# Kernel optimization log

Hardware: AMD Instinct MI355X
Metric: run time of the kernel (lower is better)

## Reference

```python
import jax, jax.numpy as jnp
import numpy as np

N, T1, T2 = 150000, 30000, 8192
E1, E2 = 400000, 160000
F_IN, F_HID, F_OUT = 512, 256, 20


def setup_inputs() -> dict:
    key = jax.random.key(0)
    ks = jax.random.split(key, 10)
    return {
        "x": jax.random.normal(ks[0], (N, F_IN), dtype=jnp.float32),
        "src1": jax.random.randint(ks[1], (E1,), 0, N, dtype=jnp.int32),
        "dst1": jax.random.randint(ks[2], (E1,), 0, T1, dtype=jnp.int32),
        "src2": jax.random.randint(ks[3], (E2,), 0, T1, dtype=jnp.int32),
        "dst2": jax.random.randint(ks[4], (E2,), 0, T2, dtype=jnp.int32),
        "Wl1": jax.random.normal(ks[5], (F_HID, F_IN), dtype=jnp.float32) * 0.05,
        "bl1": jnp.zeros((F_HID,), dtype=jnp.float32),
        "Wr1": jax.random.normal(ks[6], (F_HID, F_IN), dtype=jnp.float32) * 0.05,
        "Wl2": jax.random.normal(ks[7], (F_OUT, F_HID), dtype=jnp.float32) * 0.05,
        "bl2": jnp.zeros((F_OUT,), dtype=jnp.float32),
        "Wr2": jax.random.normal(ks[8], (F_OUT, F_HID), dtype=jnp.float32) * 0.05,
    }


def _sage_conv(x_src, x_tgt, src, dst, num_tgt, Wl, bl, Wr):
    # PyG SAGEConv (mean aggr, root_weight=True, bias on lin_l):
    # out = lin_l(mean_{j in N(i)} x_src[j]) + lin_r(x_tgt[i])
    msg = x_src[src]                                                  # [E, F]
    agg = jax.ops.segment_sum(msg, dst, num_segments=num_tgt)        # [T, F]
    cnt = jax.ops.segment_sum(jnp.ones((src.shape[0],), x_src.dtype), dst,
                              num_segments=num_tgt)                  # [T]
    mean = agg / jnp.maximum(cnt, 1.0)[:, None]
    return mean @ Wl.T + bl + x_tgt @ Wr.T


def reference(x, src1, dst1, src2, dst2, Wl1, bl1, Wr1, Wl2, bl2, Wr2):
    # Layer 1: [N, F_IN] -> [T1, F_HID], relu (eval mode: no dropout)
    h = _sage_conv(x, x[:T1], src1, dst1, T1, Wl1, bl1, Wr1)
    h = jax.nn.relu(h)
    # Layer 2: [T1, F_HID] -> [T2, F_OUT]
    out = _sage_conv(h, h[:T2], src2, dst2, T2, Wl2, bl2, Wr2)
    return jax.nn.log_softmax(out, axis=-1)
```

## Files before the change

kernel.cpp:

```cpp
#include <hip/hip_runtime.h>
#include <math.h>

constexpr int T1N  = 30000;
constexpr int T2N  = 8192;
constexpr int FIN  = 512;
constexpr int FHID = 256;
constexpr int FOUT = 20;
constexpr int NPAD = 32;

typedef short bf16x8 __attribute__((ext_vector_type(8)));
typedef short bf16x4 __attribute__((ext_vector_type(4)));
typedef float f32x4  __attribute__((ext_vector_type(4)));

__device__ __forceinline__ short f2bf(float f) {
    unsigned u = __float_as_uint(f);
    u += 0x7fff + ((u >> 16) & 1);
    return (short)(u >> 16);
}
__device__ __forceinline__ float bf2f(short s) {
    return __uint_as_float(((unsigned)(unsigned short)s) << 16);
}

__device__ __forceinline__ void gload16(const void* g, void* l) {
    __builtin_amdgcn_global_load_lds(
        (const __attribute__((address_space(1))) void*)g,
        (__attribute__((address_space(3))) void*)l, 16, 0, 0);
}

__global__ void count_both(const int* __restrict__ dst1, const int* __restrict__ dst2,
        int* __restrict__ cnt1, int* __restrict__ cnt2, int E1, int E2) {
    int i = blockIdx.x * blockDim.x + threadIdx.x;
    int stride = gridDim.x * blockDim.x;
    int tot = E1 + E2;
    for (; i < tot; i += stride) {
        if (i < E1) atomicAdd(&cnt1[dst1[i]], 1);
        else        atomicAdd(&cnt2[dst2[i - E1]], 1);
    }
}

__global__ __launch_bounds__(1024) void scan_both(
        const int* __restrict__ cnt1, int* __restrict__ rs1, int* __restrict__ cur1,
        const int* __restrict__ cnt2, int* __restrict__ rs2, int* __restrict__ cur2) {
    const int* cnt = (blockIdx.x == 0) ? cnt1 : cnt2;
    int* rs  = (blockIdx.x == 0) ? rs1  : rs2;
    int* cur = (blockIdx.x == 0) ? cur1 : cur2;
    int T    = (blockIdx.x == 0) ? T1N  : T2N;
    __shared__ int wsum[16];
    int tid = threadIdx.x;
    int lane = tid & 63, wid = tid >> 6;
    int carry = 0;
    for (int base = 0; base < T; base += 4096) {
        int i = base + tid * 4;
        int4 v = make_int4(0, 0, 0, 0);
        if (i + 3 < T) v = *(const int4*)(cnt + i);
        else {
            if (i     < T) v.x = cnt[i];
            if (i + 1 < T) v.y = cnt[i + 1];
            if (i + 2 < T) v.z = cnt[i + 2];
        }
        int tsum = v.x + v.y + v.z + v.w;
        int s = tsum;
        #pragma unroll
        for (int off = 1; off < 64; off <<= 1) {
            int t = __shfl_up(s, off, 64);
            if (lane >= off) s += t;
        }
        if (lane == 63) wsum[wid] = s;
        __syncthreads();
        if (wid == 0) {
            int w = (lane < 16) ? wsum[lane] : 0;
            #pragma unroll
            for (int off = 1; off < 16; off <<= 1) {
                int t = __shfl_up(w, off, 64);
                if (lane >= off) w += t;
            }
            if (lane < 16) wsum[lane] = w;
        }
        __syncthreads();
        int e0 = s - tsum + (wid > 0 ? wsum[wid - 1] : 0) + carry;
        int e1 = e0 + v.x, e2 = e1 + v.y, e3 = e2 + v.z;
        if (i + 3 < T) {
            *(int4*)(rs + i)  = make_int4(e0, e1, e2, e3);
            *(int4*)(cur + i) = make_int4(e0, e1, e2, e3);
        } else {
            if (i     < T) { rs[i]     = e0; cur[i]     = e0; }
            if (i + 1 < T) { rs[i + 1] = e1; cur[i + 1] = e1; }
            if (i + 2 < T) { rs[i + 2] = e2; cur[i + 2] = e2; }
        }
        int total = wsum[15];
        __syncthreads();
        carry += total;
    }
    if (tid == 0) rs[T] = carry;
}

__global__ void scatter_both(const int* __restrict__ src1, const int* __restrict__ dst1,
        const int* __restrict__ src2, const int* __restrict__ dst2,
        int* __restrict__ cur1, int* __restrict__ cur2,
        int* __restrict__ ss1, int* __restrict__ ss2, int E1, int E2) {
    int i = blockIdx.x * blockDim.x + threadIdx.x;
    int stride = gridDim.x * blockDim.x;
    int tot = E1 + E2;
    for (; i < tot; i += stride) {
        if (i < E1) {
            int pos = atomicAdd(&cur1[dst1[i]], 1);
            ss1[pos] = src1[i];
        } else {
            int j = i - E1;
            int pos = atomicAdd(&cur2[dst2[j]], 1);
            ss2[pos] = src2[j];
        }
    }
}

__global__ void convert_x_full(const float* __restrict__ x, short* __restrict__ xbf, long n8) {
    long i = ((long)blockIdx.x * blockDim.x + threadIdx.x);
    if (i >= n8) return;
    const float* p = x + i * 8;
    float4 v0 = *(const float4*)p;
    float4 v1 = *(const float4*)(p + 4);
    bf16x8 o;
    o[0] = f2bf(v0.x); o[1] = f2bf(v0.y); o[2] = f2bf(v0.z); o[3] = f2bf(v0.w);
    o[4] = f2bf(v1.x); o[5] = f2bf(v1.y); o[6] = f2bf(v1.z); o[7] = f2bf(v1.w);
    *(bf16x8*)(xbf + i * 8) = o;
}

__global__ void convert_w_all(const float* __restrict__ Wl1, const float* __restrict__ Wr1,
        const float* __restrict__ Wl2, short* __restrict__ Wl1bf,
        short* __restrict__ Wr1bf, short* __restrict__ Wl2pad) {
    int i = (blockIdx.x * blockDim.x + threadIdx.x) * 8;
    const int S1 = FHID * FIN;
    if (i < S1) {
        const float* sp = Wl1 + i;
        float4 v0 = *(const float4*)sp, v1 = *(const float4*)(sp + 4);
        bf16x8 o;
        o[0]=f2bf(v0.x); o[1]=f2bf(v0.y); o[2]=f2bf(v0.z); o[3]=f2bf(v0.w);
        o[4]=f2bf(v1.x); o[5]=f2bf(v1.y); o[6]=f2bf(v1.z); o[7]=f2bf(v1.w);
        *(bf16x8*)(Wl1bf + i) = o;
    } else if (i < 2 * S1) {
        const float* sp = Wr1 + (i - S1);
        float4 v0 = *(const float4*)sp, v1 = *(const float4*)(sp + 4);
        bf16x8 o;
        o[0]=f2bf(v0.x); o[1]=f2bf(v0.y); o[2]=f2bf(v0.z); o[3]=f2bf(v0.w);
        o[4]=f2bf(v1.x); o[5]=f2bf(v1.y); o[6]=f2bf(v1.z); o[7]=f2bf(v1.w);
        *(bf16x8*)(Wr1bf + (i - S1)) = o;
    } else if (i < 2 * S1 + NPAD * FHID) {
        int k = i - 2 * S1;
        int row = k >> 8;
        bf16x8 o;
        if (row < FOUT) {
            const float* sp = Wl2 + (size_t)row * FHID + (k & 255);
            float4 v0 = *(const float4*)sp, v1 = *(const float4*)(sp + 4);
            o[0]=f2bf(v0.x); o[1]=f2bf(v0.y); o[2]=f2bf(v0.z); o[3]=f2bf(v0.w);
            o[4]=f2bf(v1.x); o[5]=f2bf(v1.y); o[6]=f2bf(v1.z); o[7]=f2bf(v1.w);
        } else {
            o = (bf16x8)(short)0;
        }
        *(bf16x8*)(Wl2pad + k) = o;
    }
}

template <int MODE>
__global__ __launch_bounds__(256, 2) void gemm_l1(
        const short* __restrict__ A, const short* __restrict__ W,
        const float* __restrict__ bias, void* __restrict__ outv, int M) {
    __shared__ short As[2][128 * 32];
    __shared__ short Bs[2][256 * 32];
    int tid = threadIdx.x;
    int wid = tid >> 6, lane = tid & 63;
    int brow = blockIdx.x * 128;
    int wr = (wid >> 1) * 64, wc = (wid & 1) * 128;

    f32x4 acc[4][8] = {};
    int kgrp = lane >> 4;
    int r16 = lane & 15;

    auto stage = [&](int buf, int kt) {
        #pragma unroll
        for (int c2 = 0; c2 < 2; ++c2) {
            int q = wid + c2 * 4;
            int c = q * 64 + lane;
            int row = c >> 2;
            int sl = (c & 3) ^ ((row ^ (row >> 2)) & 3);
            int gr = brow + row; if (gr > M - 1) gr = M - 1;
            gload16(A + (size_t)gr * 512 + kt + sl * 8, (char*)As[buf] + q * 1024);
        }
        #pragma unroll
        for (int c2 = 0; c2 < 4; ++c2) {
            int q = wid + c2 * 4;
            int c = q * 64 + lane;
            int row = c >> 2;
            int sl = (c & 3) ^ ((row ^ (row >> 2)) & 3);
            gload16(W + (size_t)row * 512 + kt + sl * 8, (char*)Bs[buf] + q * 1024);
        }
    };

    stage(0, 0);
    __syncthreads();

    int cur = 0;
    for (int kt = 0; kt < 512; kt += 32) {
        if (kt + 32 < 512) stage(cur ^ 1, kt + 32);

        bf16x8 af[4], bfr[8];
        #pragma unroll
        for (int m = 0; m < 4; ++m) {
            int row = wr + m * 16 + r16;
            int sl = kgrp ^ ((row ^ (row >> 2)) & 3);
            af[m] = *(const bf16x8*)((const char*)As[cur] + row * 64 + sl * 16);
        }
        #pragma unroll
        for (int n = 0; n < 8; ++n) {
            int row = wc + n * 16 + r16;
            int sl = kgrp ^ ((row ^ (row >> 2)) & 3);
            bfr[n] = *(const bf16x8*)((const char*)Bs[cur] + row * 64 + sl * 16);
        }
        #pragma unroll
        for (int m = 0; m < 4; ++m)
            #pragma unroll
            for (int n = 0; n < 8; ++n)
                acc[m][n] = __builtin_amdgcn_mfma_f32_16x16x32_bf16(
                        af[m], bfr[n], acc[m][n], 0, 0, 0);

        __syncthreads();
        cur ^= 1;
    }

    int g4 = lane >> 4;
    #pragma unroll
    for (int n = 0; n < 8; ++n) {
        int col = wc + n * 16 + r16;
        float bv = (MODE == 1) ? bias[col] : 0.f;
        #pragma unroll
        for (int m = 0; m < 4; ++m) {
            #pragma unroll
            for (int r = 0; r < 4; ++r) {
                int row = brow + wr + m * 16 + g4 * 4 + r;
                if (row < M) {
                    if (MODE == 0)
                        ((short*)outv)[(size_t)row * 256 + col] = f2bf(acc[m][n][r]);
                    else
                        ((float*)outv)[(size_t)row * 256 + col] = acc[m][n][r] + bv;
                }
            }
        }
    }
}

__global__ void agg1_kernel(const short* __restrict__ y, const int* __restrict__ ss,
        const int* __restrict__ rs, const float* __restrict__ hr,
        float* __restrict__ h, short* __restrict__ hbf, int T) {
    int gw = (int)((blockIdx.x * (size_t)blockDim.x + threadIdx.x) >> 6);
    int lane = threadIdx.x & 63;
    if (gw >= T) return;
    int j0 = rs[gw], j1 = rs[gw + 1];
    float a[4] = {};
    for (int j = j0; j < j1; ++j) {
        int s = ss[j];
        bf16x4 v = *(const bf16x4*)(y + (size_t)s * FHID + lane * 4);
        a[0] += bf2f(v[0]); a[1] += bf2f(v[1]); a[2] += bf2f(v[2]); a[3] += bf2f(v[3]);
    }
    int d = j1 - j0;
    float inv = 1.0f / (float)(d > 1 ? d : 1);
    float4 hv = *(const float4*)(hr + (size_t)gw * FHID + lane * 4);
    float o0 = fmaxf(a[0] * inv + hv.x, 0.f);
    float o1 = fmaxf(a[1] * inv + hv.y, 0.f);
    float o2 = fmaxf(a[2] * inv + hv.z, 0.f);
    float o3 = fmaxf(a[3] * inv + hv.w, 0.f);
    *(float4*)(h + (size_t)gw * FHID + lane * 4) = make_float4(o0, o1, o2, o3);
    bf16x4 ob; ob[0] = f2bf(o0); ob[1] = f2bf(o1); ob[2] = f2bf(o2); ob[3] = f2bf(o3);
    *(bf16x4*)(hbf + (size_t)gw * FHID + lane * 4) = ob;
}

__global__ __launch_bounds__(128, 2) void gemm_z(
        const short* __restrict__ A, const short* __restrict__ W,
        float* __restrict__ z, int M) {
    __shared__ short As[2][128 * 32];
    __shared__ short Bs[2][32 * 32];
    int tid = threadIdx.x;
    int wid = tid >> 6, lane = tid & 63;
    int brow = blockIdx.x * 128;
    int wr = wid * 64;

    f32x4 acc[4][2] = {};
    int kgrp = lane >> 4;
    int r16 = lane & 15;

    auto stage = [&](int buf, int kt) {
        #pragma unroll
        for (int c2 = 0; c2 < 4; ++c2) {
            int q = wid + c2 * 2;
            int c = q * 64 + lane;
            int row = c >> 2;
            int sl = (c & 3) ^ ((row ^ (row >> 2)) & 3);
            int gr = brow + row; if (gr > M - 1) gr = M - 1;
            gload16(A + (size_t)gr * 256 + kt + sl * 8, (char*)As[buf] + q * 1024);
        }
        {
            int q = wid;
            int c = q * 64 + lane;
            int row = c >> 2;
            int sl = (c & 3) ^ ((row ^ (row >> 2)) & 3);
            gload16(W + (size_t)row * 256 + kt + sl * 8, (char*)Bs[buf] + q * 1024);
        }
    };

    stage(0, 0);
    __syncthreads();

    int cur = 0;
    for (int kt = 0; kt < 256; kt += 32) {
        if (kt + 32 < 256) stage(cur ^ 1, kt + 32);

        bf16x8 af[4], bfr[2];
        #pragma unroll
        for (int m = 0; m < 4; ++m) {
            int row = wr + m * 16 + r16;
            int sl = kgrp ^ ((row ^ (row >> 2)) & 3);
            af[m] = *(const bf16x8*)((const char*)As[cur] + row * 64 + sl * 16);
        }
        #pragma unroll
        for (int n = 0; n < 2; ++n) {
            int row = n * 16 + r16;
            int sl = kgrp ^ ((row ^ (row >> 2)) & 3);
            bfr[n] = *(const bf16x8*)((const char*)Bs[cur] + row * 64 + sl * 16);
        }
        #pragma unroll
        for (int m = 0; m < 4; ++m)
            #pragma unroll
            for (int n = 0; n < 2; ++n)
                acc[m][n] = __builtin_amdgcn_mfma_f32_16x16x32_bf16(
                        af[m], bfr[n], acc[m][n], 0, 0, 0);

        __syncthreads();
        cur ^= 1;
    }

    int g4 = lane >> 4;
    #pragma unroll
    for (int n = 0; n < 2; ++n) {
        int col = n * 16 + r16;
        #pragma unroll
        for (int m = 0; m < 4; ++m) {
            #pragma unroll
            for (int r = 0; r < 4; ++r) {
                int row = brow + wr + m * 16 + g4 * 4 + r;
                if (row < M)
                    z[(size_t)row * NPAD + col] = acc[m][n][r];
            }
        }
    }
}

__global__ void agg2z_kernel(const float* __restrict__ z, const int* __restrict__ ss,
        const int* __restrict__ rs, float* __restrict__ mz, int T) {
    int gw = (int)((blockIdx.x * (size_t)blockDim.x + threadIdx.x) >> 6);
    int lane = threadIdx.x & 63;
    int t = gw * 2 + (lane >> 5);
    int c = lane & 31;
    if (t >= T) return;
    int j0 = rs[t], j1 = rs[t + 1];
    float a = 0.f;
    for (int j = j0; j < j1; ++j)
        a += z[(size_t)ss[j] * NPAD + c];
    int d = j1 - j0;
    mz[(size_t)t * NPAD + c] = a / (float)(d > 1 ? d : 1);
}

__global__ __launch_bounds__(256) void lsm_kernel(const float* __restrict__ mz,
        const float* __restrict__ h, const float* __restrict__ Wr,
        const float* __restrict__ bias, float* __restrict__ out) {
    __shared__ float Wrs[FOUT * FHID];
    int tid = threadIdx.x;
    for (int i = tid; i < FOUT * FHID / 4; i += 256)
        ((float4*)Wrs)[i] = ((const float4*)Wr)[i];
    __syncthreads();

    int row = blockIdx.x * 4 + (tid >> 6);
    int lane = tid & 63;
    if (row >= T2N) return;

    float acc[FOUT];
    #pragma unroll
    for (int o = 0; o < FOUT; ++o) acc[o] = 0.f;

    const float* hrow = h + (size_t)row * FHID;
    #pragma unroll
    for (int kk = 0; kk < 4; ++kk) {
        int k = lane + kk * 64;
        float hv = hrow[k];
        #pragma unroll
        for (int o = 0; o < FOUT; ++o)
            acc[o] = fmaf(hv, Wrs[o * FHID + k], acc[o]);
    }
    #pragma unroll
    for (int o = 0; o < FOUT; ++o)
        #pragma unroll
        for (int off = 32; off > 0; off >>= 1)
            acc[o] += __shfl_down(acc[o], off, 64);

    if (lane == 0) {
        float mx = -1e30f;
        #pragma unroll
        for (int o = 0; o < FOUT; ++o) {
            acc[o] += mz[(size_t)row * NPAD + o] + bias[o];
            mx = fmaxf(mx, acc[o]);
        }
        float s = 0.f;
        #pragma unroll
        for (int o = 0; o < FOUT; ++o) s += expf(acc[o] - mx);
        float lse = mx + logf(s);
        float* op = out + (size_t)row * FOUT;
        #pragma unroll
        for (int o = 0; o < FOUT; ++o) op[o] = acc[o] - lse;
    }
}

extern "C" void kernel_launch(void* const* d_in, const int* in_sizes, int n_in,
                              void* d_out, int out_size, void* d_ws, size_t ws_size,
                              hipStream_t stream) {
    const float* x   = (const float*)d_in[0];
    const int* src1  = (const int*)d_in[1];
    const int* dst1  = (const int*)d_in[2];
    const int* src2  = (const int*)d_in[3];
    const int* dst2  = (const int*)d_in[4];
    const float* Wl1 = (const float*)d_in[5];
    const float* bl1 = (const float*)d_in[6];
    const float* Wr1 = (const float*)d_in[7];
    const float* Wl2 = (const float*)d_in[8];
    const float* bl2 = (const float*)d_in[9];
    const float* Wr2 = (const float*)d_in[10];
    int E1 = in_sizes[1];
    int E2 = in_sizes[3];
    int N  = in_sizes[0] / FIN;

    char* p = (char*)d_ws;
    auto alloc = [&](size_t bytes) {
        char* r = p;
        p += (bytes + 255) & ~(size_t)255;
        return r;
    };
    short* xbf    = (short*)alloc((size_t)N * FIN * 2);
    short* ybuf   = (short*)alloc((size_t)N * FHID * 2);
    float* hr     = (float*)alloc((size_t)T1N * FHID * 4);
    float* hbuf   = (float*)alloc((size_t)T1N * FHID * 4);
    short* hbf    = (short*)alloc((size_t)T1N * FHID * 2);
    float* zbuf   = (float*)alloc((size_t)T1N * NPAD * 4);
    float* mz     = (float*)alloc((size_t)T2N * NPAD * 4);
    short* Wl1bf  = (short*)alloc((size_t)FHID * FIN * 2);
    short* Wr1bf  = (short*)alloc((size_t)FHID * FIN * 2);
    short* Wl2pad = (short*)alloc((size_t)NPAD * FHID * 2);
    int* cnt1 = (int*)alloc((size_t)T1N * 4);
    int* cnt2 = (int*)alloc((size_t)T2N * 4);
    int* rs1  = (int*)alloc((size_t)(T1N + 1) * 4);
    int* cur1 = (int*)alloc((size_t)T1N * 4);
    int* ss1  = (int*)alloc((size_t)E1 * 4);
    int* rs2  = (int*)alloc((size_t)(T2N + 1) * 4);
    int* cur2 = (int*)alloc((size_t)T2N * 4);
    int* ss2  = (int*)alloc((size_t)E2 * 4);

    hipMemsetAsync(cnt1, 0, (size_t)((char*)(cnt2 + T2N) - (char*)cnt1), stream);

    count_both<<<768, 256, 0, stream>>>(dst1, dst2, cnt1, cnt2, E1, E2);
    scan_both<<<2, 1024, 0, stream>>>(cnt1, rs1, cur1, cnt2, rs2, cur2);
    scatter_both<<<768, 256, 0, stream>>>(src1, dst1, src2, dst2, cur1, cur2, ss1, ss2, E1, E2);

    convert_w_all<<<((2 * FHID * FIN + NPAD * FHID) / 8 + 255) / 256, 256, 0, stream>>>(
        Wl1, Wr1, Wl2, Wl1bf, Wr1bf, Wl2pad);
    long n8 = (long)N * FIN / 8;
    convert_x_full<<<(int)((n8 + 255) / 256), 256, 0, stream>>>(x, xbf, n8);

    gemm_l1<1><<<(T1N + 127) / 128, 256, 0, stream>>>(xbf, Wr1bf, bl1, hr, T1N);
    gemm_l1<0><<<(N + 127) / 128, 256, 0, stream>>>(xbf, Wl1bf, nullptr, ybuf, N);
    agg1_kernel<<<(T1N * 64 + 255) / 256, 256, 0, stream>>>(ybuf, ss1, rs1, hr, hbuf, hbf, T1N);

    gemm_z<<<(T1N + 127) / 128, 128, 0, stream>>>(hbf, Wl2pad, zbuf, T1N);
    agg2z_kernel<<<(T2N / 2 * 64 + 255) / 256, 256, 0, stream>>>(zbuf, ss2, rs2, mz, T2N);
    lsm_kernel<<<T2N / 4, 256, 0, stream>>>(mz, hbuf, Wr2, bl2, (float*)d_out);
}
```

Baseline: 728.3 us.

## Aggregate raw features before layer-1 GEMM and fuse both weights into one K=1024 GEMM

Layer 1 now computes the neighbour mean directly on the bf16 input features for the 30000 target rows. It then runs a single MFMA GEMM over the concatenation [mean | x_tgt] against concatenated [Wl1 | Wr1] weights, with bias and ReLU fused into the epilogue. The old path transformed all 150000 source rows by Wl1, wrote a projected buffer and gathered from it. This removes most of the layer-1 GEMM work, the projected-buffer write and a separate pass. The cost is that each edge now gathers 512-wide bf16 rows instead of 256-wide ones, doubling per-edge gather traffic.

```diff
diff --git a/kernel.cpp b/kernel.cpp
--- a/kernel.cpp
+++ b/kernel.cpp
@@ -126,26 +126,22 @@
 }
 
 __global__ void convert_w_all(const float* __restrict__ Wl1, const float* __restrict__ Wr1,
-        const float* __restrict__ Wl2, short* __restrict__ Wl1bf,
-        short* __restrict__ Wr1bf, short* __restrict__ Wl2pad) {
+        const float* __restrict__ Wl2, short* __restrict__ Wcat,
+        short* __restrict__ Wl2pad) {
     int i = (blockIdx.x * blockDim.x + threadIdx.x) * 8;
-    const int S1 = FHID * FIN;
-    if (i < S1) {
-        const float* sp = Wl1 + i;
+    const int SC = FHID * 1024;
+    if (i < SC) {
+        int n = i >> 10;
+        int k = i & 1023;
+        const float* sp = (k < 512) ? (Wl1 + (size_t)n * FIN + k)
+                                    : (Wr1 + (size_t)n * FIN + (k - 512));
         float4 v0 = *(const float4*)sp, v1 = *(const float4*)(sp + 4);
         bf16x8 o;
         o[0]=f2bf(v0.x); o[1]=f2bf(v0.y); o[2]=f2bf(v0.z); o[3]=f2bf(v0.w);
         o[4]=f2bf(v1.x); o[5]=f2bf(v1.y); o[6]=f2bf(v1.z); o[7]=f2bf(v1.w);
-        *(bf16x8*)(Wl1bf + i) = o;
-    } else if (i < 2 * S1) {
-        const float* sp = Wr1 + (i - S1);
-        float4 v0 = *(const float4*)sp, v1 = *(const float4*)(sp + 4);
-        bf16x8 o;
-        o[0]=f2bf(v0.x); o[1]=f2bf(v0.y); o[2]=f2bf(v0.z); o[3]=f2bf(v0.w);
-        o[4]=f2bf(v1.x); o[5]=f2bf(v1.y); o[6]=f2bf(v1.z); o[7]=f2bf(v1.w);
-        *(bf16x8*)(Wr1bf + (i - S1)) = o;
-    } else if (i < 2 * S1 + NPAD * FHID) {
-        int k = i - 2 * S1;
+        *(bf16x8*)(Wcat + i) = o;
+    } else if (i < SC + NPAD * FHID) {
+        int k = i - SC;
         int row = k >> 8;
         bf16x8 o;
         if (row < FOUT) {
@@ -160,38 +156,63 @@
     }
 }
 
-template <int MODE>
-__global__ __launch_bounds__(256, 2) void gemm_l1(
-        const short* __restrict__ A, const short* __restrict__ W,
-        const float* __restrict__ bias, void* __restrict__ outv, int M) {
+__global__ void agg1_kernel(const short* __restrict__ xbf, const int* __restrict__ ss,
+        const int* __restrict__ rs, short* __restrict__ meanbf, int T) {
+    int gw = (int)((blockIdx.x * (size_t)blockDim.x + threadIdx.x) >> 6);
+    int lane = threadIdx.x & 63;
+    if (gw >= T) return;
+    int j0 = rs[gw], j1 = rs[gw + 1];
+    float a[8] = {};
+    int j = j0;
+    for (; j + 1 < j1; j += 2) {
+        int s0 = ss[j], s1 = ss[j + 1];
+        bf16x8 v0 = *(const bf16x8*)(xbf + (size_t)s0 * FIN + lane * 8);
+        bf16x8 v1 = *(const bf16x8*)(xbf + (size_t)s1 * FIN + lane * 8);
+        #pragma unroll
+        for (int q = 0; q < 8; ++q) a[q] += bf2f(v0[q]) + bf2f(v1[q]);
+    }
+    if (j < j1) {
+        int s0 = ss[j];
+        bf16x8 v0 = *(const bf16x8*)(xbf + (size_t)s0 * FIN + lane * 8);
+        #pragma unroll
+        for (int q = 0; q < 8; ++q) a[q] += bf2f(v0[q]);
+    }
+    int d = j1 - j0;
+    float inv = 1.0f / (float)(d > 1 ? d : 1);
+    bf16x8 o;
+    #pragma unroll
+    for (int q = 0; q < 8; ++q) o[q] = f2bf(a[q] * inv);
+    *(bf16x8*)(meanbf + (size_t)gw * FIN + lane * 8) = o;
+}
+
+__global__ __launch_bounds__(256, 2) void gemm1_mfma(
+        const short* __restrict__ Am, const short* __restrict__ Ax,
+        const short* __restrict__ W, const float* __restrict__ bias,
+        float* __restrict__ h, short* __restrict__ hbf) {
     __shared__ short As[2][128 * 32];
-    __shared__ short Bs[2][256 * 32];
+    __shared__ short Bs[2][128 * 32];
     int tid = threadIdx.x;
     int wid = tid >> 6, lane = tid & 63;
-    int brow = blockIdx.x * 128;
-    int wr = (wid >> 1) * 64, wc = (wid & 1) * 128;
-
-    f32x4 acc[4][8] = {};
+    int brow = blockIdx.x * 128, bcol = blockIdx.y * 128;
+    int wr = (wid >> 1) * 64, wc = (wid & 1) * 64;
+
+    f32x4 acc[4][4] = {};
     int kgrp = lane >> 4;
     int r16 = lane & 15;
 
     auto stage = [&](int buf, int kt) {
+        const short* Abase = (kt < 512) ? Am : Ax;
+        int ko = kt & 511;
         #pragma unroll
         for (int c2 = 0; c2 < 2; ++c2) {
             int q = wid + c2 * 4;
             int c = q * 64 + lane;
             int row = c >> 2;
-            int sl = (c & 3) ^ ((row ^ (row >> 2)) & 3);
-            int gr = brow + row; if (gr > M - 1) gr = M - 1;
-            gload16(A + (size_t)gr * 512 + kt + sl * 8, (char*)As[buf] + q * 1024);
-        }
-        #pragma unroll
-        for (int c2 = 0; c2 < 4; ++c2) {
-            int q = wid + c2 * 4;
-            int c = q * 64 + lane;
-            int row = c >> 2;
-            int sl = (c & 3) ^ ((row ^ (row >> 2)) & 3);
-            gload16(W + (size_t)row * 512 + kt + sl * 8, (char*)Bs[buf] + q * 1024);
+            int rx = (row ^ (row >> 2)) & 3;
+            int sl = (c & 3) ^ rx;
+            int gr = brow + row; if (gr > T1N - 1) gr = T1N - 1;
+            gload16(Abase + (size_t)gr * 512 + ko + sl * 8, (char*)As[buf] + q * 1024);
+            gload16(W + (size_t)(bcol + row) * 1024 + kt + sl * 8, (char*)Bs[buf] + q * 1024);
         }
     };
 
@@ -199,10 +220,10 @@
     __syncthreads();
 
     int cur = 0;
-    for (int kt = 0; kt < 512; kt += 32) {
-        if (kt + 32 < 512) stage(cur ^ 1, kt + 32);
-
-        bf16x8 af[4], bfr[8];
+    for (int kt = 0; kt < 1024; kt += 32) {
+        if (kt + 32 < 1024) stage(cur ^ 1, kt + 32);
+
+        bf16x8 af[4], bfr[4];
         #pragma unroll
         for (int m = 0; m < 4; ++m) {
             int row = wr + m * 16 + r16;
@@ -210,7 +231,7 @@
             af[m] = *(const bf16x8*)((const char*)As[cur] + row * 64 + sl * 16);
         }
         #pragma unroll
-        for (int n = 0; n < 8; ++n) {
+        for (int n = 0; n < 4; ++n) {
             int row = wc + n * 16 + r16;
             int sl = kgrp ^ ((row ^ (row >> 2)) & 3);
             bfr[n] = *(const bf16x8*)((const char*)Bs[cur] + row * 64 + sl * 16);
@@ -218,7 +239,7 @@
         #pragma unroll
         for (int m = 0; m < 4; ++m)
             #pragma unroll
-            for (int n = 0; n < 8; ++n)
+            for (int n = 0; n < 4; ++n)
                 acc[m][n] = __builtin_amdgcn_mfma_f32_16x16x32_bf16(
                         af[m], bfr[n], acc[m][n], 0, 0, 0);
 
@@ -228,48 +249,23 @@
 
     int g4 = lane >> 4;
     #pragma unroll
-    for (int n = 0; n < 8; ++n) {
-        int col = wc + n * 16 + r16;
-        float bv = (MODE == 1) ? bias[col] : 0.f;
+    for (int n = 0; n < 4; ++n) {
+        int col = bcol + wc + n * 16 + r16;
+        float bv = bias[col];
         #pragma unroll
         for (int m = 0; m < 4; ++m) {
             #pragma unroll
             for (int r = 0; r < 4; ++r) {
                 int row = brow + wr + m * 16 + g4 * 4 + r;
-                if (row < M) {
-                    if (MODE == 0)
-                        ((short*)outv)[(size_t)row * 256 + col] = f2bf(acc[m][n][r]);
-                    else
-                        ((float*)outv)[(size_t)row * 256 + col] = acc[m][n][r] + bv;
+                if (row < T1N) {
+                    float v = acc[m][n][r] + bv;
+                    v = v > 0.f ? v : 0.f;
+                    h[(size_t)row * FHID + col] = v;
+                    hbf[(size_t)row * FHID + col] = f2bf(v);
                 }
             }
         }
     }
-}
-
-__global__ void agg1_kernel(const short* __restrict__ y, const int* __restrict__ ss,
-        const int* __restrict__ rs, const float* __restrict__ hr,
-        float* __restrict__ h, short* __restrict__ hbf, int T) {
-    int gw = (int)((blockIdx.x * (size_t)blockDim.x + threadIdx.x) >> 6);
-    int lane = threadIdx.x & 63;
-    if (gw >= T) return;
-    int j0 = rs[gw], j1 = rs[gw + 1];
-    float a[4] = {};
-    for (int j = j0; j < j1; ++j) {
-        int s = ss[j];
-        bf16x4 v = *(const bf16x4*)(y + (size_t)s * FHID + lane * 4);
-        a[0] += bf2f(v[0]); a[1] += bf2f(v[1]); a[2] += bf2f(v[2]); a[3] += bf2f(v[3]);
-    }
-    int d = j1 - j0;
-    float inv = 1.0f / (float)(d > 1 ? d : 1);
-    float4 hv = *(const float4*)(hr + (size_t)gw * FHID + lane * 4);
-    float o0 = fmaxf(a[0] * inv + hv.x, 0.f);
-    float o1 = fmaxf(a[1] * inv + hv.y, 0.f);
-    float o2 = fmaxf(a[2] * inv + hv.z, 0.f);
-    float o3 = fmaxf(a[3] * inv + hv.w, 0.f);
-    *(float4*)(h + (size_t)gw * FHID + lane * 4) = make_float4(o0, o1, o2, o3);
-    bf16x4 ob; ob[0] = f2bf(o0); ob[1] = f2bf(o1); ob[2] = f2bf(o2); ob[3] = f2bf(o3);
-    *(bf16x4*)(hbf + (size_t)gw * FHID + lane * 4) = ob;
 }
 
 __global__ __launch_bounds__(128, 2) void gemm_z(
@@ -441,14 +437,12 @@
         return r;
     };
     short* xbf    = (short*)alloc((size_t)N * FIN * 2);
-    short* ybuf   = (short*)alloc((size_t)N * FHID * 2);
-    float* hr     = (float*)alloc((size_t)T1N * FHID * 4);
+    short* meanbf = (short*)alloc((size_t)T1N * FIN * 2);
     float* hbuf   = (float*)alloc((size_t)T1N * FHID * 4);
     short* hbf    = (short*)alloc((size_t)T1N * FHID * 2);
     float* zbuf   = (float*)alloc((size_t)T1N * NPAD * 4);
     float* mz     = (float*)alloc((size_t)T2N * NPAD * 4);
-    short* Wl1bf  = (short*)alloc((size_t)FHID * FIN * 2);
-    short* Wr1bf  = (short*)alloc((size_t)FHID * FIN * 2);
+    short* Wcat   = (short*)alloc((size_t)FHID * 1024 * 2);
     short* Wl2pad = (short*)alloc((size_t)NPAD * FHID * 2);
     int* cnt1 = (int*)alloc((size_t)T1N * 4);
     int* cnt2 = (int*)alloc((size_t)T2N * 4);
@@ -465,14 +459,14 @@
     scan_both<<<2, 1024, 0, stream>>>(cnt1, rs1, cur1, cnt2, rs2, cur2);
     scatter_both<<<768, 256, 0, stream>>>(src1, dst1, src2, dst2, cur1, cur2, ss1, ss2, E1, E2);
 
-    convert_w_all<<<((2 * FHID * FIN + NPAD * FHID) / 8 + 255) / 256, 256, 0, stream>>>(
-        Wl1, Wr1, Wl2, Wl1bf, Wr1bf, Wl2pad);
+    convert_w_all<<<((FHID * 1024 + NPAD * FHID) / 8 + 255) / 256, 256, 0, stream>>>(
+        Wl1, Wr1, Wl2, Wcat, Wl2pad);
     long n8 = (long)N * FIN / 8;
     convert_x_full<<<(int)((n8 + 255) / 256), 256, 0, stream>>>(x, xbf, n8);
 
-    gemm_l1<1><<<(T1N + 127) / 128, 256, 0, stream>>>(xbf, Wr1bf, bl1, hr, T1N);
-    gemm_l1<0><<<(N + 127) / 128, 256, 0, stream>>>(xbf, Wl1bf, nullptr, ybuf, N);
-    agg1_kernel<<<(T1N * 64 + 255) / 256, 256, 0, stream>>>(ybuf, ss1, rs1, hr, hbuf, hbf, T1N);
+    agg1_kernel<<<(T1N * 64 + 255) / 256, 256, 0, stream>>>(xbf, ss1, rs1, meanbf, T1N);
+    dim3 g1((T1N + 127) / 128, FHID / 128);
+    gemm1_mfma<<<g1, 256, 0, stream>>>(meanbf, xbf, Wcat, bl1, hbuf, hbf);
 
     gemm_z<<<(T1N + 127) / 128, 128, 0, stream>>>(hbf, Wl2pad, zbuf, T1N);
     agg2z_kernel<<<(T2N / 2 * 64 + 255) / 256, 256, 0, stream>>>(zbuf, ss2, rs2, mz, T2N);
```

New measurement: 659.0 us. 1.11x faster.
